# Performance work log

Measured on AMD Instinct MI355X. Metric: run time of the kernel, lower is better.

## Reference

```python
import jax, jax.numpy as jnp
import numpy as np

VOCAB, EMB, HID, B, T = 50000, 300, 150, 256, 512

def _lstm_params(key, in_dim, hid):
    k1, k2, k3, k4 = jax.random.split(key, 4)
    s = 1.0 / np.sqrt(hid)
    return (jax.random.uniform(k1, (4 * hid, in_dim), minval=-s, maxval=s),
            jax.random.uniform(k2, (4 * hid, hid), minval=-s, maxval=s),
            jax.random.uniform(k3, (4 * hid,), minval=-s, maxval=s),
            jax.random.uniform(k4, (4 * hid,), minval=-s, maxval=s))

def setup_inputs() -> dict:
    key = jax.random.key(0)
    ks = jax.random.split(key, 16)
    emb = jax.random.normal(ks[0], (VOCAB, EMB), dtype=jnp.float32)
    emb = emb.at[0].set(0.0)  # padding_idx=0
    x = jax.random.randint(ks[1], (B, T), 0, VOCAB, dtype=jnp.int64)
    lengths = jax.random.randint(ks[2], (B,), 1, T + 1, dtype=jnp.int64)
    inp = {"x": x, "lengths": lengths, "emb": emb}
    in_dims = [EMB, HID, HID, HID]  # lstm1 layers 0,1 ; lstm2 layers 0,1
    for l in range(4):
        Wih, Whh, bih, bhh = _lstm_params(ks[3 + l], in_dims[l], HID)
        inp[f"Wih{l}"], inp[f"Whh{l}"], inp[f"bih{l}"], inp[f"bhh{l}"] = Wih, Whh, bih, bhh
    s = 1.0 / np.sqrt(HID)
    inp["fc1_w"] = jax.random.uniform(ks[8], (HID, HID), minval=-s, maxval=s)
    inp["fc1_b"] = jax.random.uniform(ks[9], (HID,), minval=-s, maxval=s)
    inp["fc2_w"] = jax.random.uniform(ks[10], (1, HID), minval=-s, maxval=s)
    inp["fc2_b"] = jax.random.uniform(ks[11], (1,), minval=-s, maxval=s)
    return inp

def _lstm_layer(x_seq, lengths, Wih, Whh, bih, bhh):
    # x_seq: [B, T, D]. Packed-sequence semantics: state updated only while t < length;
    # padded output positions are zero (matching pad_packed_sequence).
    Bsz, Tlen, _ = x_seq.shape
    hid = Whh.shape[1]
    x_proj = jnp.einsum('btd,gd->btg', x_seq, Wih) + bih + bhh  # [B,T,4H]

    def step(carry, inp):
        h, c = carry
        xg, t = inp
        gates = xg + h @ Whh.T
        i, f, g, o = jnp.split(gates, 4, axis=-1)
        i, f, o = jax.nn.sigmoid(i), jax.nn.sigmoid(f), jax.nn.sigmoid(o)
        g = jnp.tanh(g)
        c_new = f * c + i * g
        h_new = o * jnp.tanh(c_new)
        mask = (t < lengths)[:, None]
        h = jnp.where(mask, h_new, h)
        c = jnp.where(mask, c_new, c)
        out = jnp.where(mask, h_new, 0.0)
        return (h, c), out

    h0 = jnp.zeros((Bsz, hid), x_seq.dtype)
    (hT, cT), outs = jax.lax.scan(step, (h0, h0),
                                  (jnp.swapaxes(x_proj, 0, 1), jnp.arange(Tlen)))
    return jnp.swapaxes(outs, 0, 1), hT

def reference(x, lengths, emb,
              Wih0, Whh0, bih0, bhh0, Wih1, Whh1, bih1, bhh1,
              Wih2, Whh2, bih2, bhh2, Wih3, Whh3, bih3, bhh3,
              fc1_w, fc1_b, fc2_w, fc2_b):
    h = emb[x]  # [B, T, EMB] embedding lookup
    # lstm1 (2 layers)
    h, _ = _lstm_layer(h, lengths, Wih0, Whh0, bih0, bhh0)
    h, _ = _lstm_layer(h, lengths, Wih1, Whh1, bih1, bhh1)
    # lstm2 (2 layers); hn from its last layer
    h, _ = _lstm_layer(h, lengths, Wih2, Whh2, bih2, bhh2)
    _, hn = _lstm_layer(h, lengths, Wih3, Whh3, bih3, bhh3)
    z = jax.nn.relu(hn @ fc1_w.T + fc1_b)
    out = z @ fc2_w.T + fc2_b
    return out.flatten()
```

## Files before the change

kernel.cpp:

```cpp
#include <hip/hip_runtime.h>

#define HIDN 150
#define NG   600
#define NGP  640
#define TT   512
#define NBATCH 256
#define KPA  160
#define KPE  320

typedef __attribute__((ext_vector_type(8))) short bf16x8;
typedef __attribute__((ext_vector_type(4))) float f32x4;

__device__ __forceinline__ unsigned short f2bf(float v) {
    unsigned int u = __builtin_bit_cast(unsigned int, v);
    u += 0x7fffu + ((u >> 16) & 1u);
    return (unsigned short)(u >> 16);
}
__device__ __forceinline__ float bf2f(unsigned short h) {
    unsigned int u = ((unsigned int)h) << 16;
    return __builtin_bit_cast(float, u);
}

#define GLDS(gp, lp) __builtin_amdgcn_global_load_lds( \
    (const __attribute__((address_space(1))) unsigned int*)(gp), \
    (__attribute__((address_space(3))) unsigned int*)(lp), 16, 0, 0)

__device__ __forceinline__ int slot_of(int n) {
    int g = n / HIDN, u = n - g * HIDN;
    return ((u >> 4) << 6) + (g << 4) + (u & 15);
}

__global__ __launch_bounds__(256) void embprep_kernel(
    const float* __restrict__ emb,
    unsigned short* __restrict__ eh, unsigned short* __restrict__ el)
{
    int i = blockIdx.x * 256 + threadIdx.x;
    if (i >= 50000 * KPE) return;
    int v = i / KPE, k = i - v * KPE;
    float x = (k < 300) ? emb[(size_t)v * 300 + k] : 0.f;
    unsigned short hi = f2bf(x);
    eh[i] = hi;
    el[i] = f2bf(x - bf2f(hi));
}

__global__ __launch_bounds__(256) void prep_kernel(
    const float* __restrict__ Wih, const float* __restrict__ Whh,
    const float* __restrict__ bih, const float* __restrict__ bhh,
    int K, int Kp,
    unsigned short* __restrict__ Wgh, unsigned short* __restrict__ Wgl,
    float* __restrict__ Wts, float* __restrict__ bsum)
{
    int i = blockIdx.x * 256 + threadIdx.x;
    int nW = NGP * Kp;
    if (i < nW) {
        int n = i / Kp, k = i - n * Kp;
        float w = (n < NG && k < K) ? Wih[(size_t)n * K + k] : 0.f;
        unsigned short hi = f2bf(w);
        Wgh[i] = hi;
        Wgl[i] = f2bf(w - bf2f(hi));
    } else if (i < nW + HIDN * NGP) {
        int j = i - nW;
        int k = j / NGP, s = j - k * NGP;
        int u = ((s >> 6) << 4) + (s & 15);
        int g = (s >> 4) & 3;
        Wts[j] = (u < HIDN) ? Whh[(size_t)(g * HIDN + u) * HIDN + k] : 0.f;
    } else if (i < nW + HIDN * NGP + NGP) {
        int g = i - nW - HIDN * NGP;
        bsum[g] = (g < NG) ? (bih[g] + bhh[g]) : 0.f;
    }
}

__global__ __launch_bounds__(256, 2) void gemm_kernel(
    const unsigned short* __restrict__ Ah, const unsigned short* __restrict__ Al,
    const int* __restrict__ gather,
    const unsigned short* __restrict__ Eh, const unsigned short* __restrict__ El,
    int Kp,
    const unsigned short* __restrict__ Wh, const unsigned short* __restrict__ Wl,
    const float* __restrict__ bsum, const int* __restrict__ lengths,
    float* __restrict__ G,
    int b_off, int t0, int lTc)
{
    int m0 = blockIdx.x * 128;
    int n0 = blockIdx.y * 128;
    int Tcm1 = (1 << lTc) - 1;
    if (lTc >= 7) {
        int b = b_off + (m0 >> lTc);
        if (t0 + (m0 & Tcm1) >= lengths[b]) return;
    }

    __shared__ __align__(16) unsigned short Ash[128][32];
    __shared__ __align__(16) unsigned short Asl[128][32];
    __shared__ __align__(16) unsigned short Bsh[128][32];
    __shared__ __align__(16) unsigned short Bsl[128][32];

    int tid = threadIdx.x, lane = tid & 63, wave = tid >> 6;

    const unsigned short* AhB = gather ? Eh : Ah;
    const unsigned short* AlB = gather ? El : Al;
    size_t ra[2], rb[2];
    int mrow[2];
    #pragma unroll
    for (int c2 = 0; c2 < 2; ++c2) {
        int mb = wave * 32 + c2 * 16;
        mrow[c2] = mb;
        int rg = m0 + mb + (lane >> 2);
        int bb = rg >> lTc, tl = rg & Tcm1;
        ra[c2] = gather ? (size_t)gather[(b_off + bb) * TT + t0 + tl] * (size_t)Kp
                        : ((size_t)bb * TT + t0 + tl) * (size_t)Kp;
        int nr = n0 + mb + (lane >> 2);
        rb[c2] = (size_t)nr * (size_t)Kp;
    }
    int klane = (lane & 3) * 8;

    f32x4 acc[4][4];
    #pragma unroll
    for (int i = 0; i < 4; ++i)
        #pragma unroll
        for (int j = 0; j < 4; ++j) acc[i][j] = (f32x4){0.f, 0.f, 0.f, 0.f};

    int fr = (lane >> 4) * 8;
    int ml = lane & 15;
    int mbase = (wave & 1) * 64;
    int nbase = (wave >> 1) * 64;

    for (int k0 = 0; k0 < Kp; k0 += 32) {
        #pragma unroll
        for (int c2 = 0; c2 < 2; ++c2) {
            GLDS(AhB + ra[c2] + k0 + klane, &Ash[mrow[c2]][0]);
            GLDS(AlB + ra[c2] + k0 + klane, &Asl[mrow[c2]][0]);
            GLDS(Wh  + rb[c2] + k0 + klane, &Bsh[mrow[c2]][0]);
            GLDS(Wl  + rb[c2] + k0 + klane, &Bsl[mrow[c2]][0]);
        }
        __syncthreads();

        bf16x8 afh[4], afl[4], bfh[4], bfl[4];
        #pragma unroll
        for (int i = 0; i < 4; ++i) {
            afh[i] = *(const bf16x8*)&Ash[mbase + i * 16 + ml][fr];
            afl[i] = *(const bf16x8*)&Asl[mbase + i * 16 + ml][fr];
            bfh[i] = *(const bf16x8*)&Bsh[nbase + i * 16 + ml][fr];
            bfl[i] = *(const bf16x8*)&Bsl[nbase + i * 16 + ml][fr];
        }
        #pragma unroll
        for (int i = 0; i < 4; ++i)
            #pragma unroll
            for (int j = 0; j < 4; ++j)
                acc[i][j] = __builtin_amdgcn_mfma_f32_16x16x32_bf16(afh[i], bfh[j], acc[i][j], 0, 0, 0);
        #pragma unroll
        for (int i = 0; i < 4; ++i)
            #pragma unroll
            for (int j = 0; j < 4; ++j)
                acc[i][j] = __builtin_amdgcn_mfma_f32_16x16x32_bf16(afh[i], bfl[j], acc[i][j], 0, 0, 0);
        #pragma unroll
        for (int i = 0; i < 4; ++i)
            #pragma unroll
            for (int j = 0; j < 4; ++j)
                acc[i][j] = __builtin_amdgcn_mfma_f32_16x16x32_bf16(afl[i], bfh[j], acc[i][j], 0, 0, 0);
        __syncthreads();
    }

    int rq = lane >> 4;
    #pragma unroll
    for (int i = 0; i < 4; ++i) {
        int mg = m0 + mbase + i * 16 + rq * 4;
        #pragma unroll
        for (int j = 0; j < 4; ++j) {
            int ng = n0 + nbase + j * 16 + ml;
            if (ng < NG) {
                float bz = bsum[ng];
                int s = slot_of(ng);
                #pragma unroll
                for (int r = 0; r < 4; ++r)
                    G[(size_t)(mg + r) * NGP + s] = acc[i][j][r] + bz;
            }
        }
    }
}

#define REGK  32
#define TAILP 11

__global__ __launch_bounds__(640) void scan_kernel(
    const float* __restrict__ G,
    const float* __restrict__ Wt,
    const int*   __restrict__ lengths,
    unsigned short* __restrict__ Aout,
    unsigned short* __restrict__ Alout,
    float* __restrict__ hnb,
    float* __restrict__ hst, float* __restrict__ cst,
    int b_off, int t0, int Tc)
{
    __shared__ __align__(16) float h_s[2][160];
    __shared__ __align__(8) float wl2[TAILP][NGP][2];

    int tid = threadIdx.x;
    int lane = tid & 63, w = tid >> 6;
    int u_loc = lane & 15, g = (lane >> 4) & 3;
    int u = w * 16 + u_loc;
    bool own = (lane < 16) && (u < HIDN);

    int l0 = blockIdx.x;
    int b  = b_off + l0;
    int len = lengths[b];
    int tmax = min(len, t0 + Tc);

    float4 wr[REGK];
    #pragma unroll
    for (int q = 0; q < REGK; ++q) {
        wr[q].x = Wt[(4 * q + 0) * NGP + tid];
        wr[q].y = Wt[(4 * q + 1) * NGP + tid];
        wr[q].z = Wt[(4 * q + 2) * NGP + tid];
        wr[q].w = Wt[(4 * q + 3) * NGP + tid];
    }
    #pragma unroll
    for (int p = 0; p < TAILP; ++p) {
        wl2[p][tid][0] = Wt[(128 + 2 * p) * NGP + tid];
        wl2[p][tid][1] = Wt[(129 + 2 * p) * NGP + tid];
    }

    float c = 0.f;
    if (tid < 160) { h_s[0][tid] = 0.f; h_s[1][tid] = 0.f; }
    if (tid < HIDN && t0 > 0) h_s[0][tid] = hst[l0 * HIDN + tid];
    if (own && t0 > 0) c = cst[l0 * HIDN + u];

    bool isg = (g == 2);
    const float* Gbase = G + (size_t)l0 * Tc * NGP + tid;
    __syncthreads();

    int p = 0;
    float gnext = (t0 < tmax) ? Gbase[(size_t)0] : 0.f;
    for (int t = t0; t < tmax; ++t) {
        float gcur = gnext;
        if (t + 1 < tmax) gnext = Gbase[(size_t)(t + 1 - t0) * NGP];
        const float* hp = &h_s[p][0];
        float acc = 0.f;
        #pragma unroll
        for (int q = 0; q < REGK; ++q) {
            float4 h4 = *(const float4*)&hp[4 * q];
            acc += wr[q].x * h4.x; acc += wr[q].y * h4.y;
            acc += wr[q].z * h4.z; acc += wr[q].w * h4.w;
        }
        #pragma unroll
        for (int q = 0; q < TAILP; ++q) {
            float2 wp = *(const float2*)&wl2[q][tid][0];
            float2 h2 = *(const float2*)&hp[128 + 2 * q];
            acc += wp.x * h2.x; acc += wp.y * h2.y;
        }
        float a = gcur + acc;
        float bb = isg ? 2.f * a : a;
        float e  = __expf(-bb);
        float r  = 1.f / (1.f + e);
        float av = isg ? 2.f * r - 1.f : r;
        float fv = __shfl(av, u_loc + 16, 64);
        float gv = __shfl(av, u_loc + 32, 64);
        float ov = __shfl(av, u_loc + 48, 64);
        if (own) {
            float cn = fv * c + av * gv;
            float e2 = __expf(-2.f * cn);
            float th = 2.f / (1.f + e2) - 1.f;
            float hv = ov * th;
            c = cn;
            h_s[p ^ 1][u] = hv;
            if (Aout) {
                size_t off = ((size_t)l0 * TT + t) * KPA + u;
                unsigned short hi = f2bf(hv);
                Aout[off]  = hi;
                Alout[off] = f2bf(hv - bf2f(hi));
            }
            if (t == len - 1) hnb[b * HIDN + u] = hv;
        }
        __syncthreads();
        p ^= 1;
    }

    if (own) {
        hst[l0 * HIDN + u] = h_s[p][u];
        cst[l0 * HIDN + u] = c;
    }
}

__global__ __launch_bounds__(256) void head_kernel(
    const float* __restrict__ hnb, const float* __restrict__ fc1_w,
    const float* __restrict__ fc1_b, const float* __restrict__ fc2_w,
    const float* __restrict__ fc2_b, float* __restrict__ out)
{
    __shared__ float hs[HIDN];
    __shared__ float zs[HIDN];
    int b = blockIdx.x, tid = threadIdx.x;
    if (tid < HIDN) hs[tid] = hnb[b * HIDN + tid];
    __syncthreads();
    if (tid < HIDN) {
        float acc = fc1_b[tid];
        const float* wr = fc1_w + (size_t)tid * HIDN;
        #pragma unroll 5
        for (int k = 0; k < HIDN; ++k) acc += wr[k] * hs[k];
        zs[tid] = fmaxf(acc, 0.f);
    }
    __syncthreads();
    if (tid == 0) {
        float s = fc2_b[0];
        for (int k = 0; k < HIDN; ++k) s += fc2_w[k] * zs[k];
        out[b] = s;
    }
}

extern "C" void kernel_launch(void* const* d_in, const int* in_sizes, int n_in,
                              void* d_out, int out_size, void* d_ws, size_t ws_size,
                              hipStream_t stream)
{
    const int*   x       = (const int*)d_in[0];
    const int*   lengths = (const int*)d_in[1];
    const float* emb     = (const float*)d_in[2];
    const float *Wih[4], *Whh[4], *bih[4], *bhh[4];
    for (int l = 0; l < 4; ++l) {
        Wih[l] = (const float*)d_in[3 + 4 * l];
        Whh[l] = (const float*)d_in[4 + 4 * l];
        bih[l] = (const float*)d_in[5 + 4 * l];
        bhh[l] = (const float*)d_in[6 + 4 * l];
    }
    const float* fc1_w = (const float*)d_in[19];
    const float* fc1_b = (const float*)d_in[20];
    const float* fc2_w = (const float*)d_in[21];
    const float* fc2_b = (const float*)d_in[22];

    int Kl[4]  = {300, 150, 150, 150};
    int Kp[4]  = {KPE, KPA, KPA, KPA};
    size_t wgoff[4];
    size_t wgacc = 0;
    for (int l = 0; l < 4; ++l) { wgoff[l] = wgacc; wgacc += 2 * (size_t)NGP * Kp[l]; }

    size_t wf = ws_size / sizeof(float);
    const size_t WFIX = 384000 + 2560 + 38400 + 512000 + 16000000;
    int NBc = 0, Tc = 0;
    for (int nb = 256; nb >= 16; nb >>= 1) {
        for (int tc = 512; tc >= 8; tc >>= 1) {
            size_t need = WFIX + (size_t)nb * 300
                        + (size_t)nb * TT * KPA
                        + (size_t)nb * tc * NGP;
            if (need <= wf) { NBc = nb; Tc = tc; break; }
        }
        if (NBc) break;
    }
    if (!NBc) return;
    int lTc = __builtin_ctz(Tc);

    float* ws  = (float*)d_ws;
    float* Wts = ws;
    float* bsm = Wts + 384000;
    float* hnb = bsm + 2560;
    unsigned short* Wg = (unsigned short*)(hnb + 38400);
    unsigned short* embh = Wg + 1024000;
    unsigned short* embl = embh + 16000000;
    float* hst = (float*)(embl + 16000000);
    float* cst = hst + (size_t)NBc * HIDN;
    unsigned short* Ahh = (unsigned short*)(cst + (size_t)NBc * HIDN);
    unsigned short* Ahl = Ahh + (size_t)NBc * TT * KPA;
    float* G   = (float*)(Ahl + (size_t)NBc * TT * KPA);

    embprep_kernel<<<(50000 * KPE + 255) / 256, 256, 0, stream>>>(emb, embh, embl);
    for (int l = 0; l < 4; ++l) {
        int total = NGP * Kp[l] + HIDN * NGP + NGP;
        prep_kernel<<<(total + 255) / 256, 256, 0, stream>>>(
            Wih[l], Whh[l], bih[l], bhh[l], Kl[l], Kp[l],
            Wg + wgoff[l], Wg + wgoff[l] + (size_t)NGP * Kp[l],
            Wts + l * 96000, bsm + l * 640);
    }

    int nTc = TT / Tc;
    int nBc = NBATCH / NBc;
    dim3 ggrid((unsigned)(NBc * Tc / 128), 5);
    for (int bc = 0; bc < nBc; ++bc) {
        int b_off = bc * NBc;
        for (int l = 0; l < 4; ++l) {
            const unsigned short* Wh = Wg + wgoff[l];
            const unsigned short* Wl = Wh + (size_t)NGP * Kp[l];
            for (int tc = 0; tc < nTc; ++tc) {
                int t0 = tc * Tc;
                gemm_kernel<<<ggrid, 256, 0, stream>>>(
                    (l == 0) ? nullptr : Ahh, (l == 0) ? nullptr : Ahl,
                    (l == 0) ? x : nullptr, embh, embl,
                    Kp[l], Wh, Wl, bsm + l * 640, lengths, G, b_off, t0, lTc);
                scan_kernel<<<NBc, 640, 0, stream>>>(
                    G, Wts + l * 96000, lengths,
                    (l == 3) ? nullptr : Ahh, (l == 3) ? nullptr : Ahl,
                    hnb, hst, cst, b_off, t0, Tc);
            }
        }
    }
    head_kernel<<<256, 256, 0, stream>>>(hnb, fc1_w, fc1_b, fc2_w, fc2_b, (float*)d_out);
}
```

Baseline: 3.346 ms.

## Split recurrent matvec K across gate lanes with shuffle reduction in scan kernel

The recurrent h·Whh matvec is reorganized so each lane of a 16-unit group handles a quarter of K (40 columns) for all four gates of its unit, rather than the full K for one gate. Partial sums are combined with two xor shuffles. Whh is padded to 160 rows, and launch bounds request two blocks per CU so occupancy can double. Per-lane weight registers drop (128 pinned plus 8 LDS float4 rows) and the per-step LDS traffic for h changes, at the cost of extra shuffles and the LDS tail loads.

```diff
diff --git a/kernel.cpp b/kernel.cpp
--- a/kernel.cpp
+++ b/kernel.cpp
@@ -58,14 +58,14 @@
         unsigned short hi = f2bf(w);
         Wgh[i] = hi;
         Wgl[i] = f2bf(w - bf2f(hi));
-    } else if (i < nW + HIDN * NGP) {
+    } else if (i < nW + 160 * NGP) {
         int j = i - nW;
         int k = j / NGP, s = j - k * NGP;
         int u = ((s >> 6) << 4) + (s & 15);
         int g = (s >> 4) & 3;
-        Wts[j] = (u < HIDN) ? Whh[(size_t)(g * HIDN + u) * HIDN + k] : 0.f;
-    } else if (i < nW + HIDN * NGP + NGP) {
-        int g = i - nW - HIDN * NGP;
+        Wts[j] = (u < HIDN && k < HIDN) ? Whh[(size_t)(g * HIDN + u) * HIDN + k] : 0.f;
+    } else if (i < nW + 160 * NGP + NGP) {
+        int g = i - nW - 160 * NGP;
         bsum[g] = (g < NG) ? (bih[g] + bhh[g]) : 0.f;
     }
 }
@@ -177,10 +177,34 @@
     }
 }
 
-#define REGK  32
-#define TAILP 11
-
-__global__ __launch_bounds__(640) void scan_kernel(
+#define KQ   40
+#define LKK  8
+
+#define QR(X) X(0) X(1) X(2) X(3) X(4) X(5) X(6) X(7) X(8) X(9) \
+              X(10) X(11) X(12) X(13) X(14) X(15) X(16) X(17) X(18) X(19) \
+              X(20) X(21) X(22) X(23) X(24) X(25) X(26) X(27) X(28) X(29) \
+              X(30) X(31)
+
+#define DECLW(kk) float wA##kk = Wq[(kk)*NGP +  0], wB##kk = Wq[(kk)*NGP + 16], \
+                        wC##kk = Wq[(kk)*NGP + 32], wD##kk = Wq[(kk)*NGP + 48];
+#define PINW(kk)  asm volatile("" : "+v"(wA##kk), "+v"(wB##kk), "+v"(wC##kk), "+v"(wD##kk));
+#define FMAJ(j,k0,k1,k2,k3) { float4 h4 = *(const float4*)&hp[KQ*q + 4*(j)]; \
+  p0 += wA##k0*h4.x; p1 += wB##k0*h4.x; p2 += wC##k0*h4.x; p3 += wD##k0*h4.x; \
+  p0 += wA##k1*h4.y; p1 += wB##k1*h4.y; p2 += wC##k1*h4.y; p3 += wD##k1*h4.y; \
+  p0 += wA##k2*h4.z; p1 += wB##k2*h4.z; p2 += wC##k2*h4.z; p3 += wD##k2*h4.z; \
+  p0 += wA##k3*h4.w; p1 += wB##k3*h4.w; p2 += wC##k3*h4.w; p3 += wD##k3*h4.w; }
+#define FMAL(j,m0,m1,m2,m3) { float4 h4 = *(const float4*)&hp[KQ*q + 4*(j)]; \
+  float4 q0 = *(const float4*)&wl[m0][tid][0]; \
+  float4 q1 = *(const float4*)&wl[m1][tid][0]; \
+  float4 q2 = *(const float4*)&wl[m2][tid][0]; \
+  float4 q3 = *(const float4*)&wl[m3][tid][0]; \
+  p0 += q0.x*h4.x; p1 += q0.y*h4.x; p2 += q0.z*h4.x; p3 += q0.w*h4.x; \
+  p0 += q1.x*h4.y; p1 += q1.y*h4.y; p2 += q1.z*h4.y; p3 += q1.w*h4.y; \
+  p0 += q2.x*h4.z; p1 += q2.y*h4.z; p2 += q2.z*h4.z; p3 += q2.w*h4.z; \
+  p0 += q3.x*h4.w; p1 += q3.y*h4.w; p2 += q3.z*h4.w; p3 += q3.w*h4.w; }
+
+__global__ __launch_bounds__(640, 2)
+void scan_kernel(
     const float* __restrict__ G,
     const float* __restrict__ Wt,
     const int*   __restrict__ lengths,
@@ -191,11 +215,11 @@
     int b_off, int t0, int Tc)
 {
     __shared__ __align__(16) float h_s[2][160];
-    __shared__ __align__(8) float wl2[TAILP][NGP][2];
+    __shared__ __align__(16) float wl[LKK][NGP][4];
 
     int tid = threadIdx.x;
     int lane = tid & 63, w = tid >> 6;
-    int u_loc = lane & 15, g = (lane >> 4) & 3;
+    int u_loc = lane & 15, q = (lane >> 4) & 3;
     int u = w * 16 + u_loc;
     bool own = (lane < 16) && (u < HIDN);
 
@@ -204,18 +228,17 @@
     int len = lengths[b];
     int tmax = min(len, t0 + Tc);
 
-    float4 wr[REGK];
+    const float* Wq = Wt + (size_t)(KQ * q) * NGP + (tid - q * 16);
+
+    QR(DECLW)
+    QR(PINW)
+
     #pragma unroll
-    for (int q = 0; q < REGK; ++q) {
-        wr[q].x = Wt[(4 * q + 0) * NGP + tid];
-        wr[q].y = Wt[(4 * q + 1) * NGP + tid];
-        wr[q].z = Wt[(4 * q + 2) * NGP + tid];
-        wr[q].w = Wt[(4 * q + 3) * NGP + tid];
-    }
-    #pragma unroll
-    for (int p = 0; p < TAILP; ++p) {
-        wl2[p][tid][0] = Wt[(128 + 2 * p) * NGP + tid];
-        wl2[p][tid][1] = Wt[(129 + 2 * p) * NGP + tid];
+    for (int m = 0; m < LKK; ++m) {
+        wl[m][tid][0] = Wq[(32 + m) * NGP +  0];
+        wl[m][tid][1] = Wq[(32 + m) * NGP + 16];
+        wl[m][tid][2] = Wq[(32 + m) * NGP + 32];
+        wl[m][tid][3] = Wq[(32 + m) * NGP + 48];
     }
 
     float c = 0.f;
@@ -223,7 +246,7 @@
     if (tid < HIDN && t0 > 0) h_s[0][tid] = hst[l0 * HIDN + tid];
     if (own && t0 > 0) c = cst[l0 * HIDN + u];
 
-    bool isg = (g == 2);
+    bool isg = (q == 2);
     const float* Gbase = G + (size_t)l0 * Tc * NGP + tid;
     __syncthreads();
 
@@ -233,20 +256,19 @@
         float gcur = gnext;
         if (t + 1 < tmax) gnext = Gbase[(size_t)(t + 1 - t0) * NGP];
         const float* hp = &h_s[p][0];
-        float acc = 0.f;
-        #pragma unroll
-        for (int q = 0; q < REGK; ++q) {
-            float4 h4 = *(const float4*)&hp[4 * q];
-            acc += wr[q].x * h4.x; acc += wr[q].y * h4.y;
-            acc += wr[q].z * h4.z; acc += wr[q].w * h4.w;
-        }
-        #pragma unroll
-        for (int q = 0; q < TAILP; ++q) {
-            float2 wp = *(const float2*)&wl2[q][tid][0];
-            float2 h2 = *(const float2*)&hp[128 + 2 * q];
-            acc += wp.x * h2.x; acc += wp.y * h2.y;
-        }
-        float a = gcur + acc;
+        float p0 = 0.f, p1 = 0.f, p2 = 0.f, p3 = 0.f;
+        FMAJ(0,0,1,2,3)    FMAJ(1,4,5,6,7)    FMAJ(2,8,9,10,11)   FMAJ(3,12,13,14,15)
+        FMAJ(4,16,17,18,19) FMAJ(5,20,21,22,23) FMAJ(6,24,25,26,27) FMAJ(7,28,29,30,31)
+        FMAL(8,0,1,2,3)    FMAL(9,4,5,6,7)
+        if      (q == 0) p0 += gcur;
+        else if (q == 1) p1 += gcur;
+        else if (q == 2) p2 += gcur;
+        else             p3 += gcur;
+        p0 += __shfl_xor(p0, 16, 64); p1 += __shfl_xor(p1, 16, 64);
+        p2 += __shfl_xor(p2, 16, 64); p3 += __shfl_xor(p3, 16, 64);
+        p0 += __shfl_xor(p0, 32, 64); p1 += __shfl_xor(p1, 32, 64);
+        p2 += __shfl_xor(p2, 32, 64); p3 += __shfl_xor(p3, 32, 64);
+        float a = (q == 0) ? p0 : (q == 1) ? p1 : (q == 2) ? p2 : p3;
         float bb = isg ? 2.f * a : a;
         float e  = __expf(-bb);
         float r  = 1.f / (1.f + e);
@@ -330,7 +352,7 @@
     for (int l = 0; l < 4; ++l) { wgoff[l] = wgacc; wgacc += 2 * (size_t)NGP * Kp[l]; }
 
     size_t wf = ws_size / sizeof(float);
-    const size_t WFIX = 384000 + 2560 + 38400 + 512000 + 16000000;
+    const size_t WFIX = 409600 + 2560 + 38400 + 512000 + 16000000;
     int NBc = 0, Tc = 0;
     for (int nb = 256; nb >= 16; nb >>= 1) {
         for (int tc = 512; tc >= 8; tc >>= 1) {
@@ -346,7 +368,7 @@
 
     float* ws  = (float*)d_ws;
     float* Wts = ws;
-    float* bsm = Wts + 384000;
+    float* bsm = Wts + 409600;
     float* hnb = bsm + 2560;
     unsigned short* Wg = (unsigned short*)(hnb + 38400);
     unsigned short* embh = Wg + 1024000;
@@ -359,11 +381,11 @@
 
     embprep_kernel<<<(50000 * KPE + 255) / 256, 256, 0, stream>>>(emb, embh, embl);
     for (int l = 0; l < 4; ++l) {
-        int total = NGP * Kp[l] + HIDN * NGP + NGP;
+        int total = NGP * Kp[l] + 160 * NGP + NGP;
         prep_kernel<<<(total + 255) / 256, 256, 0, stream>>>(
             Wih[l], Whh[l], bih[l], bhh[l], Kl[l], Kp[l],
             Wg + wgoff[l], Wg + wgoff[l] + (size_t)NGP * Kp[l],
-            Wts + l * 96000, bsm + l * 640);
+            Wts + l * 102400, bsm + l * 640);
     }
 
     int nTc = TT / Tc;
@@ -381,7 +403,7 @@
                     (l == 0) ? x : nullptr, embh, embl,
                     Kp[l], Wh, Wl, bsm + l * 640, lengths, G, b_off, t0, lTc);
                 scan_kernel<<<NBc, 640, 0, stream>>>(
-                    G, Wts + l * 96000, lengths,
+                    G, Wts + l * 102400, lengths,
                     (l == 3) ? nullptr : Ahh, (l == 3) ? nullptr : Ahl,
                     hnb, hst, cst, b_off, t0, Tc);
             }
```

After: 4.115 ms. 23.0% more time.
